# Optimization experiments

Measured on AMD Instinct MI355X. Metric: run time of the kernel, lower is better.

The kernel has to match this reference:

```python
import jax, jax.numpy as jnp
import numpy as np

N = 200_000   # hits
K = 512       # truth objects (showers)
D = 3         # clustering-space dim
Q_MIN = 1.0
REPULSION_CONTRIB = 0.5


def _oc_loss(coords, truth_indices):
    """Object-condensation attractive/repulsive loss (LLClusterCoordinates,
    3-input branch: beta fixed at 0.5, use_average_cc_pos=1, Q_MIN=1, S_B=0)."""
    n = coords.shape[0]
    tidx = truth_indices[:, 0]
    notnoise = (tidx >= 0).astype(coords.dtype)           # [N]
    seg = jnp.clip(tidx, 0, K - 1)                        # safe segment ids

    # beta_like = 0.5 everywhere -> charge q_i = arctanh(beta)^2 + Q_MIN
    beta = jnp.full((n,), 0.5, dtype=coords.dtype)
    q = jnp.arctanh(beta) ** 2 + Q_MIN                    # [N]

    # per-object condensation charge from max-beta hit
    beta_max = jax.ops.segment_max(jnp.where(tidx >= 0, beta, 0.0), seg, num_segments=K)
    obj_present = jax.ops.segment_sum(notnoise, seg, num_segments=K) > 0
    q_alpha = jnp.arctanh(jnp.clip(beta_max, 0.0, 1.0 - 1e-4)) ** 2 + Q_MIN
    q_alpha = jnp.where(obj_present, q_alpha, 0.0)        # [K] (absent objs contribute 0)

    # q-weighted average condensation-point position (use_average_cc_pos = 1.0)
    w = q * notnoise                                      # [N]
    wsum = jax.ops.segment_sum(w, seg, num_segments=K)    # [K]
    cc = jax.ops.segment_sum(coords * w[:, None], seg, num_segments=K) \
         / jnp.maximum(wsum, 1e-6)[:, None]               # [K, D]

    # pairwise squared distances hit -> condensation point  [N, K]
    d2 = jnp.sum((coords[:, None, :] - cc[None, :, :]) ** 2, axis=-1)

    # attractive: each non-noise hit pulled to its own object's cc (squared dist)
    d2_own = jnp.take_along_axis(d2, seg[:, None], axis=1)[:, 0]      # [N]
    qa_own = q_alpha[seg]                                             # [N]
    V_att = jnp.sum(q * qa_own * d2_own * notnoise) / n

    # repulsive hinge: every hit pushed from every OTHER object's cc
    d = jnp.sqrt(d2 + 1e-6)
    rep_all = jnp.sum(q_alpha[None, :] * jax.nn.relu(1.0 - d), axis=1)          # [N]
    d_own = jnp.sqrt(d2_own + 1e-6)
    rep_own = qa_own * jax.nn.relu(1.0 - d_own) * notnoise                      # [N]
    V_rep = jnp.sum(q * (rep_all - rep_own)) / n

    return (1.0 - REPULSION_CONTRIB) * V_att + REPULSION_CONTRIB * V_rep


def setup_inputs() -> dict:
    key = jax.random.key(0)
    k1, k2 = jax.random.split(key)
    coords = jax.random.normal(k1, (N, D), dtype=jnp.float32)
    truth_indices = jax.random.randint(k2, (N, 1), 0, K).astype(jnp.int32)
    row_splits = jnp.array([0, N], dtype=jnp.int32)
    return {"coords": coords, "truth_indices": truth_indices, "row_splits": row_splits}


def reference(coords, truth_indices, row_splits):
    # single event: row_splits == [0, N]; loss is per-event so segments suffice
    return _oc_loss(coords, truth_indices)
```

## Files before the change

### kernel.cpp

```cpp
#include <hip/hip_runtime.h>
#include <math.h>

#define K_CL 512
#define K_Q  128
#define QC 1.3017372f


__global__ __launch_bounds__(256) void oc_bins(
    const float* __restrict__ coords, const int* __restrict__ tidx,
    float* __restrict__ bins, float* __restrict__ out, int n) {
    __shared__ float sb[K_CL * 4];
    for (int j = threadIdx.x; j < K_CL * 4; j += 256) sb[j] = 0.0f;
    if (blockIdx.x == 0 && threadIdx.x == 0) *out = 0.0f;
    __syncthreads();
    int stride = gridDim.x * 256;
    for (int i = blockIdx.x * 256 + threadIdx.x; i < n; i += stride) {
        int t = tidx[i];
        if (t >= 0) {
            int seg = t < K_CL ? t : K_CL - 1;
            float x = coords[3 * i + 0];
            float y = coords[3 * i + 1];
            float z = coords[3 * i + 2];
            atomicAdd(&sb[4 * seg + 0], QC);
            atomicAdd(&sb[4 * seg + 1], QC * x);
            atomicAdd(&sb[4 * seg + 2], QC * y);
            atomicAdd(&sb[4 * seg + 3], QC * z);
        }
    }
    __syncthreads();
    for (int j = threadIdx.x; j < K_CL * 4; j += 256) {
        float v = sb[j];
        if (v != 0.0f) unsafeAtomicAdd(&bins[j], v);
    }
}

__global__ __launch_bounds__(256) void oc_main(
    const float* __restrict__ coords, const int* __restrict__ tidx,
    const float4* __restrict__ bins4, float* __restrict__ out,
    int n, int q, float scale) {
    __shared__ float4 sa[K_Q];
    int kb = blockIdx.x & 3;
    int pb = blockIdx.x >> 2;
    int klo = kb * K_Q;
    if (threadIdx.x < K_Q) {
        int k = threadIdx.x;
        float4 b = bins4[klo + k];
        float w = b.x;
        float inv = 1.0f / fmaxf(w, 1e-6f);
        float cx = b.y * inv, cy = b.z * inv, cz = b.w * inv;
        float c2 = cx * cx + cy * cy + cz * cz;
        sa[k] = (w > 0.5f) ? make_float4(-2.0f * cx, -2.0f * cy, -2.0f * cz, c2)
                           : make_float4(0.0f, 0.0f, 0.0f, 1e30f);
    }
    __syncthreads();

    int g = pb * 256 + threadIdx.x;
    bool gv = g < q;
    int i0 = g, i1 = g + q, i2 = g + 2 * q, i3 = g + 3 * q;
    bool v0 = gv, v1 = gv && i1 < n, v2 = gv && i2 < n, v3 = gv && i3 < n;

    float x0=0.f,y0=0.f,z0=0.f; int t0=-1;
    float x1=0.f,y1=0.f,z1=0.f; int t1=-1;
    float x2=0.f,y2=0.f,z2=0.f; int t2=-1;
    float x3=0.f,y3=0.f,z3=0.f; int t3=-1;
    if (v0) { x0=coords[3*i0]; y0=coords[3*i0+1]; z0=coords[3*i0+2]; t0=tidx[i0]; }
    if (v1) { x1=coords[3*i1]; y1=coords[3*i1+1]; z1=coords[3*i1+2]; t1=tidx[i1]; }
    if (v2) { x2=coords[3*i2]; y2=coords[3*i2+1]; z2=coords[3*i2+2]; t2=tidx[i2]; }
    if (v3) { x3=coords[3*i3]; y3=coords[3*i3+1]; z3=coords[3*i3+2]; t3=tidx[i3]; }

    float sp0 = fmaf(x0,x0,fmaf(y0,y0,z0*z0));
    float sp1 = fmaf(x1,x1,fmaf(y1,y1,z1*z1));
    float sp2 = fmaf(x2,x2,fmaf(y2,y2,z2*z2));
    float sp3 = fmaf(x3,x3,fmaf(y3,y3,z3*z3));
    float se0 = sp0 + 1e-6f;
    float se1 = sp1 + 1e-6f;
    float se2 = sp2 + 1e-6f;
    float se3 = sp3 + 1e-6f;

    float r0 = 0.0f, r1 = 0.0f, r2 = 0.0f, r3 = 0.0f;
    #pragma unroll 4
    for (int k = 0; k < K_Q; ++k) {
        float4 a = sa[k];
        float e0 = fmaf(x0, a.x, fmaf(y0, a.y, fmaf(z0, a.z, se0 + a.w)));
        float e1 = fmaf(x1, a.x, fmaf(y1, a.y, fmaf(z1, a.z, se1 + a.w)));
        float e2 = fmaf(x2, a.x, fmaf(y2, a.y, fmaf(z2, a.z, se2 + a.w)));
        float e3 = fmaf(x3, a.x, fmaf(y3, a.y, fmaf(z3, a.z, se3 + a.w)));
        r0 += fminf(__builtin_amdgcn_sqrtf(e0), 1.0f);
        r1 += fminf(__builtin_amdgcn_sqrtf(e1), 1.0f);
        r2 += fminf(__builtin_amdgcn_sqrtf(e2), 1.0f);
        r3 += fminf(__builtin_amdgcn_sqrtf(e3), 1.0f);
    }

    int s0 = (t0<0)?-1:(t0<K_CL?t0:K_CL-1);
    int s1 = (t1<0)?-1:(t1<K_CL?t1:K_CL-1);
    int s2 = (t2<0)?-1:(t2<K_CL?t2:K_CL-1);
    int s3 = (t3<0)?-1:(t3<K_CL?t3:K_CL-1);
    int l0 = s0-klo, l1 = s1-klo, l2 = s2-klo, l3 = s3-klo;
    bool o0 = (l0>=0)&&(l0<K_Q);
    bool o1 = (l1>=0)&&(l1<K_Q);
    bool o2 = (l2>=0)&&(l2<K_Q);
    bool o3 = (l3>=0)&&(l3<K_Q);
    float4 a0 = o0 ? sa[l0] : make_float4(0.f,0.f,0.f,0.f);
    float4 a1 = o1 ? sa[l1] : make_float4(0.f,0.f,0.f,0.f);
    float4 a2 = o2 ? sa[l2] : make_float4(0.f,0.f,0.f,0.f);
    float4 a3 = o3 ? sa[l3] : make_float4(0.f,0.f,0.f,0.f);
    float d2o0 = fmaxf(sp0 + a0.w + fmaf(x0,a0.x,fmaf(y0,a0.y,z0*a0.z)), 0.0f);
    float d2o1 = fmaxf(sp1 + a1.w + fmaf(x1,a1.x,fmaf(y1,a1.y,z1*a1.z)), 0.0f);
    float d2o2 = fmaxf(sp2 + a2.w + fmaf(x2,a2.x,fmaf(y2,a2.y,z2*a2.z)), 0.0f);
    float d2o3 = fmaxf(sp3 + a3.w + fmaf(x3,a3.x,fmaf(y3,a3.y,z3*a3.z)), 0.0f);
    float tt0 = fmaxf(1.0f - __builtin_amdgcn_sqrtf(d2o0 + 1e-6f), 0.0f);
    float tt1 = fmaxf(1.0f - __builtin_amdgcn_sqrtf(d2o1 + 1e-6f), 0.0f);
    float tt2 = fmaxf(1.0f - __builtin_amdgcn_sqrtf(d2o2 + 1e-6f), 0.0f);
    float tt3 = fmaxf(1.0f - __builtin_amdgcn_sqrtf(d2o3 + 1e-6f), 0.0f);

    float c0 = (o0 ? (d2o0 - tt0) : 0.0f) + ((float)K_Q - r0);
    float c1 = (o1 ? (d2o1 - tt1) : 0.0f) + ((float)K_Q - r1);
    float c2 = (o2 ? (d2o2 - tt2) : 0.0f) + ((float)K_Q - r2);
    float c3 = (o3 ? (d2o3 - tt3) : 0.0f) + ((float)K_Q - r3);
    float contrib = (v0?c0:0.0f) + (v1?c1:0.0f) + (v2?c2:0.0f) + (v3?c3:0.0f);

    #pragma unroll
    for (int off = 32; off > 0; off >>= 1)
        contrib += __shfl_down(contrib, off, 64);
    __shared__ float wpart[4];
    int wid = threadIdx.x >> 6;
    int lane = threadIdx.x & 63;
    if (lane == 0) wpart[wid] = contrib;
    __syncthreads();
    if (threadIdx.x == 0) {
        float s = wpart[0] + wpart[1] + wpart[2] + wpart[3];
        unsafeAtomicAdd(out, s * scale);
    }
}

extern "C" void kernel_launch(void* const* d_in, const int* in_sizes, int n_in,
                              void* d_out, int out_size, void* d_ws, size_t ws_size,
                              hipStream_t stream) {
    const float* coords = (const float*)d_in[0];
    const int* tidx = (const int*)d_in[1];
    int n = in_sizes[1];
    float* ws = (float*)d_ws;
    float* out = (float*)d_out;

    oc_bins<<<256, 256, 0, stream>>>(coords, tidx, ws, out, n);

    int q = (n + 3) / 4;
    int pblocks = (q + 255) / 256;
    float scale = 0.5f * QC * QC / (float)n;
    oc_main<<<pblocks * 4, 256, 0, stream>>>(
        coords, tidx, (const float4*)ws, out, n, q, scale);
}
```

Baseline: 98.35 us.

## Replace global atomic bin accumulation with per-block partials reduced in main kernel

The binning kernel now runs on a fixed set of blocks that each write their private per-object sums to a workspace slice instead of atomically adding into shared global bins. Every main-kernel block then sums the partials for its object quarter before computing condensation points. This removes global atomics and any dependence on a pre-zeroed workspace, at the cost of fewer binning blocks and redundant partial reductions in every main block.

```diff
diff --git a/kernel.cpp b/kernel.cpp
--- a/kernel.cpp
+++ b/kernel.cpp
@@ -3,18 +3,22 @@
 
 #define K_CL 512
 #define K_Q  128
+#define NB   32
 #define QC 1.3017372f
 
 
 __global__ __launch_bounds__(256) void oc_bins(
     const float* __restrict__ coords, const int* __restrict__ tidx,
-    float* __restrict__ bins, float* __restrict__ out, int n) {
-    __shared__ float sb[K_CL * 4];
+    float4* __restrict__ partial, float* __restrict__ out, int n) {
+    __shared__ float4 sb4[K_CL];
+    float* sb = (float*)sb4;
     for (int j = threadIdx.x; j < K_CL * 4; j += 256) sb[j] = 0.0f;
     if (blockIdx.x == 0 && threadIdx.x == 0) *out = 0.0f;
     __syncthreads();
-    int stride = gridDim.x * 256;
-    for (int i = blockIdx.x * 256 + threadIdx.x; i < n; i += stride) {
+    int chunk = (n + NB - 1) / NB;
+    int lo = blockIdx.x * chunk;
+    int hi = lo + chunk; if (hi > n) hi = n;
+    for (int i = lo + threadIdx.x; i < hi; i += 256) {
         int t = tidx[i];
         if (t >= 0) {
             int seg = t < K_CL ? t : K_CL - 1;
@@ -28,31 +32,44 @@
         }
     }
     __syncthreads();
-    for (int j = threadIdx.x; j < K_CL * 4; j += 256) {
-        float v = sb[j];
-        if (v != 0.0f) unsafeAtomicAdd(&bins[j], v);
-    }
+    partial[blockIdx.x * K_CL + threadIdx.x]       = sb4[threadIdx.x];
+    partial[blockIdx.x * K_CL + threadIdx.x + 256] = sb4[threadIdx.x + 256];
 }
 
 __global__ __launch_bounds__(256) void oc_main(
     const float* __restrict__ coords, const int* __restrict__ tidx,
-    const float4* __restrict__ bins4, float* __restrict__ out,
+    const float4* __restrict__ partial, float* __restrict__ out,
     int n, int q, float scale) {
-    __shared__ float4 sa[K_Q];
+    __shared__ float4 sbuf[256];
     int kb = blockIdx.x & 3;
     int pb = blockIdx.x >> 2;
     int klo = kb * K_Q;
+
+    {
+        int k  = threadIdx.x & 127;
+        int hh = threadIdx.x >> 7;
+        float4 acc = make_float4(0.f, 0.f, 0.f, 0.f);
+        #pragma unroll 4
+        for (int b = hh * (NB / 2); b < (hh + 1) * (NB / 2); ++b) {
+            float4 p = partial[b * K_CL + klo + k];
+            acc.x += p.x; acc.y += p.y; acc.z += p.z; acc.w += p.w;
+        }
+        sbuf[threadIdx.x] = acc;
+    }
+    __syncthreads();
     if (threadIdx.x < K_Q) {
         int k = threadIdx.x;
-        float4 b = bins4[klo + k];
-        float w = b.x;
+        float4 a = sbuf[k], b2 = sbuf[k + 128];
+        float w  = a.x + b2.x;
+        float wx = a.y + b2.y, wy = a.z + b2.z, wz = a.w + b2.w;
         float inv = 1.0f / fmaxf(w, 1e-6f);
-        float cx = b.y * inv, cy = b.z * inv, cz = b.w * inv;
+        float cx = wx * inv, cy = wy * inv, cz = wz * inv;
         float c2 = cx * cx + cy * cy + cz * cz;
-        sa[k] = (w > 0.5f) ? make_float4(-2.0f * cx, -2.0f * cy, -2.0f * cz, c2)
-                           : make_float4(0.0f, 0.0f, 0.0f, 1e30f);
+        sbuf[k] = (w > 0.5f) ? make_float4(-2.f * cx, -2.f * cy, -2.f * cz, c2)
+                             : make_float4(0.f, 0.f, 0.f, 1e30f);
     }
     __syncthreads();
+    const float4* sa = sbuf;
 
     int g = pb * 256 + threadIdx.x;
     bool gv = g < q;
@@ -139,14 +156,14 @@
     const float* coords = (const float*)d_in[0];
     const int* tidx = (const int*)d_in[1];
     int n = in_sizes[1];
-    float* ws = (float*)d_ws;
+    float4* partial = (float4*)d_ws;
     float* out = (float*)d_out;
 
-    oc_bins<<<256, 256, 0, stream>>>(coords, tidx, ws, out, n);
+    oc_bins<<<NB, 256, 0, stream>>>(coords, tidx, partial, out, n);
 
     int q = (n + 3) / 4;
     int pblocks = (q + 255) / 256;
     float scale = 0.5f * QC * QC / (float)n;
     oc_main<<<pblocks * 4, 256, 0, stream>>>(
-        coords, tidx, (const float4*)ws, out, n, q, scale);
+        coords, tidx, partial, out, n, q, scale);
 }
```

Measured after the change: 119.5 us. +21.5%, slower.
